# Optimization experiments

Measured on AMD Instinct MI355X. Metric: run time of the kernel, lower is better.

## Reference

```python
import jax, jax.numpy as jnp
import numpy as np

B, NIN, D = 2048, 64, 128
N_LCB, N_FMB, RANK = 32, 32, 24
DIM_HIDDEN = 1024
N_OUT = N_LCB + N_FMB  # == NIN -> identity residual
MAX_VAL = 1.0
EPS_LN_FMB_MIN, EPS_LN_FMB_MAX = 1e-11, 1e7
KERAS_LN_EPS = 1e-3


def setup_inputs() -> dict:
    key = jax.random.key(0)
    ks = jax.random.split(key, 9)
    def w(k, shape, fan):
        return (jax.random.normal(k, shape, jnp.float32) / np.sqrt(fan)).astype(jnp.float32)
    return {
        "x": jax.random.normal(ks[0], (B, NIN, D), jnp.float32),
        "noise": jax.random.uniform(ks[1], (B, N_OUT, D), jnp.float32),
        "w_lcb": w(ks[2], (NIN, N_LCB), NIN),
        "w_rank": w(ks[3], (NIN, RANK), NIN),
        "w1": w(ks[4], (NIN * RANK, DIM_HIDDEN), NIN * RANK),
        "w2": w(ks[5], (DIM_HIDDEN, DIM_HIDDEN), DIM_HIDDEN),
        "w3": w(ks[6], (DIM_HIDDEN, N_FMB * D), DIM_HIDDEN),
        "gamma": jnp.ones((D,), jnp.float32),
        "beta": jnp.zeros((D,), jnp.float32),
    }


def _forward(x, noise, w_lcb, w_rank, w1, w2, w3, gamma, beta):
    # ---- LinearCompressBlock: Dense over feature (emb-count) axis ----
    lcb = jnp.einsum("bnd,nm->bmd", x, w_lcb)  # (B, N_LCB, D)

    # ---- FactorizationMachineBlock ----
    # rank_layer on transposed input: (B, D, NIN) @ (NIN, RANK)
    r = jnp.einsum("bnd,nr->bdr", x, w_rank)          # (B, D, RANK)
    fm = jnp.einsum("bnd,bdr->bnr", x, r)             # (B, NIN, RANK)
    fm = fm.reshape(fm.shape[0], NIN * RANK)
    # custom LayerNorm (no affine, clipped std)
    mu = jnp.mean(fm, axis=-1, keepdims=True)
    cen = fm - mu
    std = jnp.sqrt(jnp.mean(cen * cen, axis=-1, keepdims=True))
    std = jnp.clip(std, EPS_LN_FMB_MIN, EPS_LN_FMB_MAX)
    fm = cen / std
    # MLP: 2 hidden relu layers + linear out, dropout=0 / inference
    h = jax.nn.relu(fm @ w1)
    h = jax.nn.relu(h @ w2)
    fmb = (h @ w3).reshape(-1, N_FMB, D)              # (B, N_FMB, D)

    out = jnp.concatenate((fmb, lcb), axis=1)          # (B, N_OUT, D)
    residual = x                                        # NIN == N_OUT -> identity

    safe = jnp.clip(out, -MAX_VAL, MAX_VAL)
    a = jnp.abs(safe)
    c = lambda t: jnp.clip(t, -MAX_VAL, MAX_VAL)

    # conv term: reshape to (B, N, D//8, 8), 1x1 conv with all-ones (8->8)
    # filter == group-sum broadcast back over the 8 lanes
    g = safe.reshape(safe.shape[0], N_OUT, D // 8, 8)
    conv = jnp.broadcast_to(g.sum(-1, keepdims=True), g.shape).reshape(safe.shape)

    extra = (
        c(jnp.log(a + 1.0))
        + c(jax.lax.rsqrt(a + 1.0))
        + c(jax.nn.softmax(safe, axis=-1))
        + c(jnp.tanh(safe))
        + c(jnp.where(safe >= 0, safe, 0.2 * safe))          # leaky_relu alpha=0.2
        + c(jnp.exp(safe))
        + c(jax.nn.softplus(safe))
        + c(jnp.log1p(a))
        + jnp.zeros_like(safe)                               # zeros_like term
        + c(jnp.round(safe))
        + jnp.ones_like(safe)                                # pow(a+eps, 0) == 1
        + c(jnp.sign(safe))
        + c(jnp.prod(safe, axis=-1, keepdims=True))
        + c(jnp.isnan(safe).astype(jnp.float32))
        + c((~(safe < 0)).astype(jnp.float32))
        + c((safe != 0).astype(jnp.float32))
        + c((safe >= 0).astype(jnp.float32))
        + c(safe.astype(jnp.int8).astype(jnp.float32))       # bitwise_and(x,x)==x after int8 cast
        + c(jnp.max(safe, axis=-1, keepdims=True))
        + c(safe + safe)                                     # add_n([safe, safe])
        + c(safe + safe)                                     # raw Add
        + 7.0 * safe                                         # slice/split-concat/merge/einsum/squeeze/pad/stack identities (|safe|<=1 so clip no-op)
        + c(jnp.where(safe > 0.5, -1.0, safe))               # tensor_scatter_nd_update
        + c(conv)
        + c(noise)                                           # tf.random.uniform (deterministic input)
        + c(jnp.arange(D, dtype=jnp.float32))                # broadcast over last axis
        + c(jnp.sum(safe[0] * safe[0], axis=-1))[None, :, None]  # DiagPart(matmul(safe[0], safe[0]^T))
    )

    pre = out + residual + 1e-10 * extra
    # keras LayerNormalization(axis=-1), default epsilon=1e-3
    m = jnp.mean(pre, axis=-1, keepdims=True)
    v = jnp.mean(jnp.square(pre - m), axis=-1, keepdims=True)
    return (pre - m) * jax.lax.rsqrt(v + KERAS_LN_EPS) * gamma + beta


def reference(x, noise, w_lcb, w_rank, w1, w2, w3, gamma, beta):
    return _forward(x, noise, w_lcb, w_rank, w1, w2, w3, gamma, beta)
```

## Files before the change

### kernel.cpp

```cpp
#include <hip/hip_runtime.h>


typedef _Float16 half8_t __attribute__((ext_vector_type(8)));
typedef _Float16 half4_t __attribute__((ext_vector_type(4)));
typedef float floatx4 __attribute__((ext_vector_type(4)));

#define B_SZ 2048
#define NIN 64
#define D_SZ 128
#define RANK 24
#define FMK (NIN * RANK)
#define HID 1024
#define NFMB_D (32 * 128)
#define ROW_F (NIN * D_SZ)

__device__ __forceinline__ void wg_barrier() {
  asm volatile("s_waitcnt lgkmcnt(0)" ::: "memory");
  __builtin_amdgcn_sched_barrier(0);
  __builtin_amdgcn_s_barrier();
  __builtin_amdgcn_sched_barrier(0);
}

__global__ __launch_bounds__(256) void transpose_cast_all(
    const float* __restrict__ w1, const float* __restrict__ w2,
    const float* __restrict__ w3, const float* __restrict__ w_rank,
    const float* __restrict__ w_lcb, _Float16* __restrict__ w1t,
    _Float16* __restrict__ w2t, _Float16* __restrict__ w3t,
    _Float16* __restrict__ wr16, _Float16* __restrict__ wl16) {
  __shared__ float tile[32][33];
  int bid = blockIdx.x;
  if (bid == 48 * 32 + 32 * 32 + 32 * 128) {
    const int t = threadIdx.x;
#pragma unroll
    for (int k = 0; k < 8; k++) {
      int i = t + k * 256;
      int j = i >> 6, n = i & 63;
      wr16[i] = (_Float16)(j < RANK ? w_rank[n * RANK + j] : 0.f);
      wl16[i] = (_Float16)w_lcb[n * 32 + j];
    }
    return;
  }
  const float* w;
  _Float16* wt;
  int K, N, kt;
  if (bid < 48 * 32) {
    w = w1; wt = w1t; K = FMK; N = HID; kt = 48;
  } else if (bid < 48 * 32 + 32 * 32) {
    bid -= 48 * 32;
    w = w2; wt = w2t; K = HID; N = HID; kt = 32;
  } else {
    bid -= 48 * 32 + 32 * 32;
    w = w3; wt = w3t; K = HID; N = NFMB_D; kt = 32;
  }
  const int tk = (bid % kt) * 32;
  const int tn = (bid / kt) * 32;
  const int tx = threadIdx.x & 31;
  const int ty = threadIdx.x >> 5;
#pragma unroll
  for (int i = 0; i < 4; i++) {
    int k = ty + i * 8;
    tile[k][tx] = w[(size_t)(tk + k) * N + (tn + tx)];
  }
  __syncthreads();
#pragma unroll
  for (int i = 0; i < 4; i++) {
    int n = ty + i * 8;
    wt[(size_t)(tn + n) * K + (tk + tx)] = (_Float16)tile[tx][n];
  }
}

#define STX 72
#define STN 136
__global__ __launch_bounds__(256, 3) void front_kernel(
    const float* __restrict__ x, const _Float16* __restrict__ wr16,
    const _Float16* __restrict__ wl16, const float* __restrict__ gamma,
    const float* __restrict__ beta, _Float16* __restrict__ fmn,
    float* __restrict__ out) {
  constexpr int XT_OFF = 0;
  constexpr int X16_OFF = 18432;
  constexpr int RT_OFF = X16_OFF + 17408;
  constexpr int RED_OFF = RT_OFF + 8704;
  __shared__ __align__(16) char smem[RED_OFF + 32];
  __shared__ float2 lstat[32][4];
  _Float16* xT = (_Float16*)(smem + XT_OFF);
  _Float16* x16 = (_Float16*)(smem + X16_OFF);
  _Float16* rT = (_Float16*)(smem + RT_OFF);
  float* redbuf = (float*)(smem + RED_OFF);
  _Float16* fmn_s = (_Float16*)(smem + RT_OFF);

  const int b = blockIdx.x, t = threadIdx.x;
  const int lane = t & 63;
  const int w = __builtin_amdgcn_readfirstlane(t >> 6);
  const int q = lane >> 4, ln = lane & 15;

  half8_t ar[2][2], al[2][2];
#pragma unroll
  for (int k = 0; k < 2; k++)
#pragma unroll
    for (int mi = 0; mi < 2; mi++) {
      ar[k][mi] = *(const half8_t*)&wr16[(mi * 16 + ln) * 64 + k * 32 + q * 8];
      al[k][mi] = *(const half8_t*)&wl16[(mi * 16 + ln) * 64 + k * 32 + q * 8];
    }

  const float4* xg4 = (const float4*)(x + (size_t)b * ROW_F);
#pragma unroll
  for (int hh = 0; hh < 2; hh++) {
    int bb = t + hh * 256;
    int n0 = (bb >> 5) * 4;
    int bd = bb & 31;
    int d0 = bd * 4;
    float4 L0 = xg4[(n0 + 0) * 32 + bd];
    float4 L1 = xg4[(n0 + 1) * 32 + bd];
    float4 L2 = xg4[(n0 + 2) * 32 + bd];
    float4 L3 = xg4[(n0 + 3) * 32 + bd];
    *(half4_t*)&x16[(n0 + 0) * STN + d0] =
        half4_t{(_Float16)L0.x, (_Float16)L0.y, (_Float16)L0.z, (_Float16)L0.w};
    *(half4_t*)&x16[(n0 + 1) * STN + d0] =
        half4_t{(_Float16)L1.x, (_Float16)L1.y, (_Float16)L1.z, (_Float16)L1.w};
    *(half4_t*)&x16[(n0 + 2) * STN + d0] =
        half4_t{(_Float16)L2.x, (_Float16)L2.y, (_Float16)L2.z, (_Float16)L2.w};
    *(half4_t*)&x16[(n0 + 3) * STN + d0] =
        half4_t{(_Float16)L3.x, (_Float16)L3.y, (_Float16)L3.z, (_Float16)L3.w};
    *(half4_t*)&xT[(d0 + 0) * STX + n0] =
        half4_t{(_Float16)L0.x, (_Float16)L1.x, (_Float16)L2.x, (_Float16)L3.x};
    *(half4_t*)&xT[(d0 + 1) * STX + n0] =
        half4_t{(_Float16)L0.y, (_Float16)L1.y, (_Float16)L2.y, (_Float16)L3.y};
    *(half4_t*)&xT[(d0 + 2) * STX + n0] =
        half4_t{(_Float16)L0.z, (_Float16)L1.z, (_Float16)L2.z, (_Float16)L3.z};
    *(half4_t*)&xT[(d0 + 3) * STX + n0] =
        half4_t{(_Float16)L0.w, (_Float16)L1.w, (_Float16)L2.w, (_Float16)L3.w};
  }
  __syncthreads();

  floatx4 r_acc[2][2] = {};
  floatx4 l_acc[2][2] = {};
#pragma unroll
  for (int k = 0; k < 2; k++) {
    half8_t bfrag[2];
#pragma unroll
    for (int ni = 0; ni < 2; ni++)
      bfrag[ni] =
          *(const half8_t*)&xT[((2 * w + ni) * 16 + ln) * STX + k * 32 + q * 8];
#pragma unroll
    for (int mi = 0; mi < 2; mi++)
#pragma unroll
      for (int ni = 0; ni < 2; ni++) {
        r_acc[mi][ni] = __builtin_amdgcn_mfma_f32_16x16x32_f16(
            ar[k][mi], bfrag[ni], r_acc[mi][ni], 0, 0, 0);
        l_acc[mi][ni] = __builtin_amdgcn_mfma_f32_16x16x32_f16(
            al[k][mi], bfrag[ni], l_acc[mi][ni], 0, 0, 0);
      }
  }
#pragma unroll
  for (int mi = 0; mi < 2; mi++)
#pragma unroll
    for (int ni = 0; ni < 2; ni++)
#pragma unroll
      for (int rr = 0; rr < 4; rr++)
        rT[(mi * 16 + q * 4 + rr) * STN + (2 * w + ni) * 16 + ln] =
            (_Float16)r_acc[mi][ni][rr];
  __syncthreads();

  floatx4 f_acc[2] = {};
#pragma unroll
  for (int k = 0; k < 4; k++) {
    half8_t af = *(const half8_t*)&x16[(w * 16 + ln) * STN + k * 32 + q * 8];
#pragma unroll
    for (int nj = 0; nj < 2; nj++) {
      half8_t bf = *(const half8_t*)&rT[(nj * 16 + ln) * STN + k * 32 + q * 8];
      f_acc[nj] =
          __builtin_amdgcn_mfma_f32_16x16x32_f16(af, bf, f_acc[nj], 0, 0, 0);
    }
  }
  float s = 0.f, s2 = 0.f;
#pragma unroll
  for (int rr = 0; rr < 4; rr++) {
    float v = f_acc[0][rr];
    s += v;
    s2 += v * v;
    float v1 = (ln < 8) ? f_acc[1][rr] : 0.f;
    s += v1;
    s2 += v1 * v1;
  }
#pragma unroll
  for (int off = 1; off < 64; off <<= 1) {
    s += __shfl_xor(s, off);
    s2 += __shfl_xor(s2, off);
  }
  if (lane == 0) {
    redbuf[w * 2] = s;
    redbuf[w * 2 + 1] = s2;
  }
  __syncthreads();
  s = redbuf[0] + redbuf[2] + redbuf[4] + redbuf[6];
  s2 = redbuf[1] + redbuf[3] + redbuf[5] + redbuf[7];
  const float mu = s * (1.f / FMK);
  float var = s2 * (1.f / FMK) - mu * mu;
  var = var > 0.f ? var : 0.f;
  float sd = sqrtf(var);
  sd = sd < 1e-11f ? 1e-11f : (sd > 1e7f ? 1e7f : sd);
  const float inv = 1.f / sd;

#pragma unroll
  for (int nj = 0; nj < 2; nj++) {
    int j = nj * 16 + ln;
    if (j < RANK) {
#pragma unroll
      for (int rr = 0; rr < 4; rr++)
        fmn_s[(w * 16 + q * 4 + rr) * RANK + j] =
            (_Float16)((f_acc[nj][rr] - mu) * inv);
    }
  }

  const int d0 = (2 * w) * 16 + ln;
  const int d1 = d0 + 16;
  const float g0 = gamma[d0], g1 = gamma[d1];
  const float be0 = beta[d0], be1 = beta[d1];
  float lv0[2][4], lv1[2][4];
  float sw[2][4], s2w[2][4];
#pragma unroll
  for (int mi = 0; mi < 2; mi++)
#pragma unroll
    for (int rr = 0; rr < 4; rr++) {
      int m = mi * 16 + q * 4 + rr;
      float v0 = l_acc[mi][0][rr] + (float)x16[(32 + m) * STN + d0];
      float v1 = l_acc[mi][1][rr] + (float)x16[(32 + m) * STN + d1];
      lv0[mi][rr] = v0;
      lv1[mi][rr] = v1;
      sw[mi][rr] = v0 + v1;
      s2w[mi][rr] = v0 * v0 + v1 * v1;
    }
#pragma unroll
  for (int off = 1; off < 16; off <<= 1) {
#pragma unroll
    for (int mi = 0; mi < 2; mi++)
#pragma unroll
      for (int rr = 0; rr < 4; rr++) {
        sw[mi][rr] += __shfl_xor(sw[mi][rr], off);
        s2w[mi][rr] += __shfl_xor(s2w[mi][rr], off);
      }
  }
  if (ln == 0) {
#pragma unroll
    for (int mi = 0; mi < 2; mi++)
#pragma unroll
      for (int rr = 0; rr < 4; rr++)
        lstat[mi * 16 + q * 4 + rr][w] = float2{sw[mi][rr], s2w[mi][rr]};
  }
  __syncthreads();

  half8_t* fg = (half8_t*)(fmn + (size_t)b * FMK);
  if (t < FMK / 8) fg[t] = ((const half8_t*)fmn_s)[t];
  float* ob = out + (size_t)b * ROW_F;
#pragma unroll
  for (int mi = 0; mi < 2; mi++)
#pragma unroll
    for (int rr = 0; rr < 4; rr++) {
      int m = mi * 16 + q * 4 + rr;
      float2 p0 = lstat[m][0], p1 = lstat[m][1];
      float2 p2 = lstat[m][2], p3 = lstat[m][3];
      float S = p0.x + p1.x + p2.x + p3.x;
      float S2 = p0.y + p1.y + p2.y + p3.y;
      float mean = S * (1.f / 128.f);
      float varr = S2 * (1.f / 128.f) - mean * mean;
      float rstd = rsqrtf(varr + 1e-3f);
      ob[(32 + m) * 128 + d0] = (lv0[mi][rr] - mean) * rstd * g0 + be0;
      ob[(32 + m) * 128 + d1] = (lv1[mi][rr] - mean) * rstd * g1 + be1;
    }
}

template <bool RELU>
__global__ __launch_bounds__(256, 2) void gemm_bt(
    const _Float16* __restrict__ A, const _Float16* __restrict__ Bt,
    _Float16* __restrict__ C, int M, int N, int K) {
  constexpr int LDT = 40;
  __shared__ __align__(16) _Float16 As[2][64 * LDT];
  __shared__ __align__(16) _Float16 Bs[2][64 * LDT];
  const int m0 = blockIdx.x * 64;
  const int n0 = blockIdx.y * 64;
  const int t = threadIdx.x;
  const int wave = t >> 6, lane = t & 63;
  const int wr = wave >> 1, wc = wave & 1;
  const int q = lane >> 4, ln = lane & 15;
  const int srow = t >> 2;
  const int skc = t & 3;
  const _Float16* gA = A + (size_t)(m0 + srow) * K + skc * 8;
  const _Float16* gB = Bt + (size_t)(n0 + srow) * K + skc * 8;
  const int ldsw = srow * LDT + skc * 8;
  const int nT = K / 32;

  floatx4 acc[2][2] = {};

  uint4 rax = *(const uint4*)gA;
  uint4 rbx = *(const uint4*)gB;
  *(uint4*)&As[0][ldsw] = rax;
  *(uint4*)&Bs[0][ldsw] = rbx;
  uint4 ray = *(const uint4*)(gA + 32);
  uint4 rby = *(const uint4*)(gB + 32);
  rax = *(const uint4*)(gA + 64);
  rbx = *(const uint4*)(gB + 64);
  wg_barrier();

  for (int tp = 0;;) {
    if (tp + 1 < nT) {
      *(uint4*)&As[1][ldsw] = ray;
      *(uint4*)&Bs[1][ldsw] = rby;
    }
    half8_t af[2], bf[2];
#pragma unroll
    for (int i = 0; i < 2; i++) {
      af[i] = *(const half8_t*)&As[0][(wr * 32 + i * 16 + ln) * LDT + q * 8];
      bf[i] = *(const half8_t*)&Bs[0][(wc * 32 + i * 16 + ln) * LDT + q * 8];
    }
    if (tp + 3 < nT) {
      ray = *(const uint4*)(gA + (tp + 3) * 32);
      rby = *(const uint4*)(gB + (tp + 3) * 32);
    }
#pragma unroll
    for (int i = 0; i < 2; i++)
#pragma unroll
      for (int j = 0; j < 2; j++)
        acc[i][j] = __builtin_amdgcn_mfma_f32_16x16x32_f16(af[i], bf[j],
                                                           acc[i][j], 0, 0, 0);
    if (tp + 1 >= nT) break;
    wg_barrier();
    if (tp + 2 < nT) {
      *(uint4*)&As[0][ldsw] = rax;
      *(uint4*)&Bs[0][ldsw] = rbx;
    }
#pragma unroll
    for (int i = 0; i < 2; i++) {
      af[i] = *(const half8_t*)&As[1][(wr * 32 + i * 16 + ln) * LDT + q * 8];
      bf[i] = *(const half8_t*)&Bs[1][(wc * 32 + i * 16 + ln) * LDT + q * 8];
    }
    if (tp + 4 < nT) {
      rax = *(const uint4*)(gA + (tp + 4) * 32);
      rbx = *(const uint4*)(gB + (tp + 4) * 32);
    }
#pragma unroll
    for (int i = 0; i < 2; i++)
#pragma unroll
      for (int j = 0; j < 2; j++)
        acc[i][j] = __builtin_amdgcn_mfma_f32_16x16x32_f16(af[i], bf[j],
                                                           acc[i][j], 0, 0, 0);
    tp += 2;
    if (tp >= nT) break;
    wg_barrier();
  }

#pragma unroll
  for (int i = 0; i < 2; i++) {
#pragma unroll
    for (int r = 0; r < 4; r++) {
      size_t row = (size_t)(m0 + wr * 32 + i * 16 + q * 4 + r);
      _Float16* crow = C + row * N + n0 + wc * 32 + ln;
#pragma unroll
      for (int j = 0; j < 2; j++) {
        float v = acc[i][j][r];
        if (RELU) v = v > 0.f ? v : 0.f;
        crow[j * 16] = (_Float16)v;
      }
    }
  }
}

__global__ __launch_bounds__(256, 2) void gemm_ln(
    const _Float16* __restrict__ A, const _Float16* __restrict__ Bt,
    const float* __restrict__ x, const float* __restrict__ gamma,
    const float* __restrict__ beta, float* __restrict__ out) {
  constexpr int LDT = 40;
  constexpr int K = HID;
  constexpr int nT = K / 32;
  __shared__ __align__(16) _Float16 As[2][128 * LDT];
  __shared__ __align__(16) _Float16 Bs[2][128 * LDT];
  __shared__ float2 rowst[128][2];
  const int m0 = blockIdx.x * 128;
  const int c = blockIdx.y;
  const int n0 = c * 128;
  const int t = threadIdx.x;
  const int wave = t >> 6, lane = t & 63;
  const int wr = wave >> 1, wc = wave & 1;
  const int q = lane >> 4, ln = lane & 15;
  const int srow = t >> 2;
  const int skc = t & 3;
  const _Float16* gA0 = A + (size_t)(m0 + srow) * K + skc * 8;
  const _Float16* gA1 = gA0 + (size_t)64 * K;
  const _Float16* gB0 = Bt + (size_t)(n0 + srow) * K + skc * 8;
  const _Float16* gB1 = gB0 + (size_t)64 * K;
  const int ldsw = srow * LDT + skc * 8;

  floatx4 acc[4][4] = {};

  uint4 raX0 = *(const uint4*)gA0, raX1 = *(const uint4*)gA1;
  uint4 rbX0 = *(const uint4*)gB0, rbX1 = *(const uint4*)gB1;
  *(uint4*)&As[0][ldsw] = raX0;
  *(uint4*)&As[0][64 * LDT + ldsw] = raX1;
  *(uint4*)&Bs[0][ldsw] = rbX0;
  *(uint4*)&Bs[0][64 * LDT + ldsw] = rbX1;
  uint4 raY0 = *(const uint4*)(gA0 + 32), raY1 = *(const uint4*)(gA1 + 32);
  uint4 rbY0 = *(const uint4*)(gB0 + 32), rbY1 = *(const uint4*)(gB1 + 32);
  raX0 = *(const uint4*)(gA0 + 64);
  raX1 = *(const uint4*)(gA1 + 64);
  rbX0 = *(const uint4*)(gB0 + 64);
  rbX1 = *(const uint4*)(gB1 + 64);

  float xp[4][4][4];
#pragma unroll
  for (int i = 0; i < 4; i++)
#pragma unroll
    for (int r = 0; r < 4; r++) {
      const int row = wr * 64 + i * 16 + q * 4 + r;
      const float* xr = x + (size_t)(m0 + row) * ROW_F + n0 + wc * 64 + ln;
#pragma unroll
      for (int j = 0; j < 4; j++) xp[i][r][j] = xr[j * 16];
    }

  wg_barrier();

  for (int tp = 0;;) {
    if (tp + 1 < nT) {
      *(uint4*)&As[1][ldsw] = raY0;
      *(uint4*)&As[1][64 * LDT + ldsw] = raY1;
      *(uint4*)&Bs[1][ldsw] = rbY0;
      *(uint4*)&Bs[1][64 * LDT + ldsw] = rbY1;
    }
    half8_t af[4], bf[4];
#pragma unroll
    for (int i = 0; i < 4; i++)
      af[i] = *(const half8_t*)&As[0][(wr * 64 + i * 16 + ln) * LDT + q * 8];
#pragma unroll
    for (int j = 0; j < 4; j++)
      bf[j] = *(const half8_t*)&Bs[0][(wc * 64 + j * 16 + ln) * LDT + q * 8];
    if (tp + 3 < nT) {
      raY0 = *(const uint4*)(gA0 + (tp + 3) * 32);
      raY1 = *(const uint4*)(gA1 + (tp + 3) * 32);
      rbY0 = *(const uint4*)(gB0 + (tp + 3) * 32);
      rbY1 = *(const uint4*)(gB1 + (tp + 3) * 32);
    }
#pragma unroll
    for (int i = 0; i < 4; i++)
#pragma unroll
      for (int j = 0; j < 4; j++)
        acc[i][j] = __builtin_amdgcn_mfma_f32_16x16x32_f16(af[i], bf[j],
                                                           acc[i][j], 0, 0, 0);
    if (tp + 1 >= nT) break;
    wg_barrier();
    if (tp + 2 < nT) {
      *(uint4*)&As[0][ldsw] = raX0;
      *(uint4*)&As[0][64 * LDT + ldsw] = raX1;
      *(uint4*)&Bs[0][ldsw] = rbX0;
      *(uint4*)&Bs[0][64 * LDT + ldsw] = rbX1;
    }
#pragma unroll
    for (int i = 0; i < 4; i++)
      af[i] = *(const half8_t*)&As[1][(wr * 64 + i * 16 + ln) * LDT + q * 8];
#pragma unroll
    for (int j = 0; j < 4; j++)
      bf[j] = *(const half8_t*)&Bs[1][(wc * 64 + j * 16 + ln) * LDT + q * 8];
    if (tp + 4 < nT) {
      raX0 = *(const uint4*)(gA0 + (tp + 4) * 32);
      raX1 = *(const uint4*)(gA1 + (tp + 4) * 32);
      rbX0 = *(const uint4*)(gB0 + (tp + 4) * 32);
      rbX1 = *(const uint4*)(gB1 + (tp + 4) * 32);
    }
#pragma unroll
    for (int i = 0; i < 4; i++)
#pragma unroll
      for (int j = 0; j < 4; j++)
        acc[i][j] = __builtin_amdgcn_mfma_f32_16x16x32_f16(af[i], bf[j],
                                                           acc[i][j], 0, 0, 0);
    tp += 2;
    if (tp >= nT) break;
    wg_barrier();
  }

  float s[4][4], s2[4][4];
#pragma unroll
  for (int i = 0; i < 4; i++)
#pragma unroll
    for (int r = 0; r < 4; r++) {
      float ss = 0.f, qq = 0.f;
#pragma unroll
      for (int j = 0; j < 4; j++) {
        float v = acc[i][j][r] + xp[i][r][j];
        acc[i][j][r] = v;
        ss += v;
        qq += v * v;
      }
      s[i][r] = ss;
      s2[i][r] = qq;
    }
#pragma unroll
  for (int off = 1; off < 16; off <<= 1) {
#pragma unroll
    for (int i = 0; i < 4; i++)
#pragma unroll
      for (int r = 0; r < 4; r++) {
        s[i][r] += __shfl_xor(s[i][r], off);
        s2[i][r] += __shfl_xor(s2[i][r], off);
      }
  }
  if (ln == 0) {
#pragma unroll
    for (int i = 0; i < 4; i++)
#pragma unroll
      for (int r = 0; r < 4; r++)
        rowst[wr * 64 + i * 16 + q * 4 + r][wc] = float2{s[i][r], s2[i][r]};
  }
  __syncthreads();
  float g[4], bb[4];
#pragma unroll
  for (int j = 0; j < 4; j++) {
    g[j] = gamma[wc * 64 + j * 16 + ln];
    bb[j] = beta[wc * 64 + j * 16 + ln];
  }
#pragma unroll
  for (int i = 0; i < 4; i++)
#pragma unroll
    for (int r = 0; r < 4; r++) {
      int row = wr * 64 + i * 16 + q * 4 + r;
      float2 p0 = rowst[row][0], p1 = rowst[row][1];
      float mean = (p0.x + p1.x) * (1.f / 128.f);
      float varr = (p0.y + p1.y) * (1.f / 128.f) - mean * mean;
      float rstd = rsqrtf(varr + 1e-3f);
      float* orow = out + (size_t)(m0 + row) * ROW_F + n0 + wc * 64 + ln;
#pragma unroll
      for (int j = 0; j < 4; j++)
        orow[j * 16] = (acc[i][j][r] - mean) * rstd * g[j] + bb[j];
    }
}

extern "C" void kernel_launch(void* const* d_in, const int* in_sizes, int n_in,
                              void* d_out, int out_size, void* d_ws,
                              size_t ws_size, hipStream_t stream) {
  const float* x = (const float*)d_in[0];
  const float* w_lcb = (const float*)d_in[2];
  const float* w_rank = (const float*)d_in[3];
  const float* w1 = (const float*)d_in[4];
  const float* w2 = (const float*)d_in[5];
  const float* w3 = (const float*)d_in[6];
  const float* gamma = (const float*)d_in[7];
  const float* beta = (const float*)d_in[8];
  float* out = (float*)d_out;

  char* ws = (char*)d_ws;
  _Float16* w1t = (_Float16*)ws; ws += (size_t)HID * FMK * 2;
  _Float16* w2t = (_Float16*)ws; ws += (size_t)HID * HID * 2;
  _Float16* w3t = (_Float16*)ws; ws += (size_t)NFMB_D * HID * 2;
  _Float16* fmn = (_Float16*)ws; ws += (size_t)B_SZ * FMK * 2;
  _Float16* h1  = (_Float16*)ws; ws += (size_t)B_SZ * HID * 2;
  _Float16* wr16 = (_Float16*)ws; ws += 32 * 64 * 2;
  _Float16* wl16 = (_Float16*)ws; ws += 32 * 64 * 2;
  _Float16* h2 = fmn;

  transpose_cast_all<<<48 * 32 + 32 * 32 + 32 * 128 + 1, 256, 0, stream>>>(
      w1, w2, w3, w_rank, w_lcb, w1t, w2t, w3t, wr16, wl16);
  front_kernel<<<B_SZ, 256, 0, stream>>>(x, wr16, wl16, gamma, beta, fmn, out);
  gemm_bt<true><<<dim3(B_SZ / 64, HID / 64), 256, 0, stream>>>(
      fmn, w1t, h1, B_SZ, HID, FMK);
  gemm_bt<true><<<dim3(B_SZ / 64, HID / 64), 256, 0, stream>>>(
      h1, w2t, h2, B_SZ, HID, HID);
  gemm_ln<<<dim3(B_SZ / 128, 32), 256, 0, stream>>>(h2, w3t, x, gamma, beta, out);
}
```

Baseline: 254.8 us.

## Deepen gemm K-tile, remap blocks per XCD, and spread residual loads across loop

```diff
diff --git a/kernel.cpp b/kernel.cpp
--- a/kernel.cpp
+++ b/kernel.cpp
@@ -274,10 +274,14 @@
     const _Float16* __restrict__ A, const _Float16* __restrict__ Bt,
     _Float16* __restrict__ C, int M, int N, int K) {
   constexpr int LDT = 40;
-  __shared__ __align__(16) _Float16 As[2][64 * LDT];
-  __shared__ __align__(16) _Float16 Bs[2][64 * LDT];
-  const int m0 = blockIdx.x * 64;
-  const int n0 = blockIdx.y * 64;
+  __shared__ __align__(16) _Float16 As[2][2][64 * LDT];
+  __shared__ __align__(16) _Float16 Bs[2][2][64 * LDT];
+  const int flat = blockIdx.x + (blockIdx.y << 5);
+  const int xcd = flat & 7, sub = flat >> 3;
+  const int mb = sub & 31;
+  const int nb = (xcd << 1) | (sub >> 5);
+  const int m0 = mb * 64;
+  const int n0 = nb * 64;
   const int t = threadIdx.x;
   const int wave = t >> 6, lane = t & 63;
   const int wr = wave >> 1, wc = wave & 1;
@@ -287,62 +291,81 @@
   const _Float16* gA = A + (size_t)(m0 + srow) * K + skc * 8;
   const _Float16* gB = Bt + (size_t)(n0 + srow) * K + skc * 8;
   const int ldsw = srow * LDT + skc * 8;
-  const int nT = K / 32;
+  const int nT = K >> 6;
 
   floatx4 acc[2][2] = {};
 
-  uint4 rax = *(const uint4*)gA;
-  uint4 rbx = *(const uint4*)gB;
-  *(uint4*)&As[0][ldsw] = rax;
-  *(uint4*)&Bs[0][ldsw] = rbx;
-  uint4 ray = *(const uint4*)(gA + 32);
-  uint4 rby = *(const uint4*)(gB + 32);
-  rax = *(const uint4*)(gA + 64);
-  rbx = *(const uint4*)(gB + 64);
+  uint4 raX0 = *(const uint4*)(gA), raX1 = *(const uint4*)(gA + 32);
+  uint4 rbX0 = *(const uint4*)(gB), rbX1 = *(const uint4*)(gB + 32);
+  *(uint4*)&As[0][0][ldsw] = raX0;
+  *(uint4*)&As[0][1][ldsw] = raX1;
+  *(uint4*)&Bs[0][0][ldsw] = rbX0;
+  *(uint4*)&Bs[0][1][ldsw] = rbX1;
+  uint4 raY0 = *(const uint4*)(gA + 64), raY1 = *(const uint4*)(gA + 96);
+  uint4 rbY0 = *(const uint4*)(gB + 64), rbY1 = *(const uint4*)(gB + 96);
+  raX0 = *(const uint4*)(gA + 128);
+  raX1 = *(const uint4*)(gA + 160);
+  rbX0 = *(const uint4*)(gB + 128);
+  rbX1 = *(const uint4*)(gB + 160);
   wg_barrier();
 
   for (int tp = 0;;) {
     if (tp + 1 < nT) {
-      *(uint4*)&As[1][ldsw] = ray;
-      *(uint4*)&Bs[1][ldsw] = rby;
-    }
-    half8_t af[2], bf[2];
-#pragma unroll
-    for (int i = 0; i < 2; i++) {
-      af[i] = *(const half8_t*)&As[0][(wr * 32 + i * 16 + ln) * LDT + q * 8];
-      bf[i] = *(const half8_t*)&Bs[0][(wc * 32 + i * 16 + ln) * LDT + q * 8];
+      *(uint4*)&As[1][0][ldsw] = raY0;
+      *(uint4*)&As[1][1][ldsw] = raY1;
+      *(uint4*)&Bs[1][0][ldsw] = rbY0;
+      *(uint4*)&Bs[1][1][ldsw] = rbY1;
     }
     if (tp + 3 < nT) {
-      ray = *(const uint4*)(gA + (tp + 3) * 32);
-      rby = *(const uint4*)(gB + (tp + 3) * 32);
-    }
-#pragma unroll
-    for (int i = 0; i < 2; i++)
-#pragma unroll
-      for (int j = 0; j < 2; j++)
-        acc[i][j] = __builtin_amdgcn_mfma_f32_16x16x32_f16(af[i], bf[j],
-                                                           acc[i][j], 0, 0, 0);
+      raY0 = *(const uint4*)(gA + (tp + 3) * 64);
+      raY1 = *(const uint4*)(gA + (tp + 3) * 64 + 32);
+      rbY0 = *(const uint4*)(gB + (tp + 3) * 64);
+      rbY1 = *(const uint4*)(gB + (tp + 3) * 64 + 32);
+    }
+#pragma unroll
+    for (int kc = 0; kc < 2; kc++) {
+      half8_t af[2], bf[2];
+#pragma unroll
+      for (int i = 0; i < 2; i++) {
+        af[i] = *(const half8_t*)&As[0][kc][(wr * 32 + i * 16 + ln) * LDT + q * 8];
+        bf[i] = *(const half8_t*)&Bs[0][kc][(wc * 32 + i * 16 + ln) * LDT + q * 8];
+      }
+#pragma unroll
+      for (int i = 0; i < 2; i++)
+#pragma unroll
+        for (int j = 0; j < 2; j++)
+          acc[i][j] = __builtin_amdgcn_mfma_f32_16x16x32_f16(af[i], bf[j],
+                                                             acc[i][j], 0, 0, 0);
+    }
     if (tp + 1 >= nT) break;
     wg_barrier();
     if (tp + 2 < nT) {
-      *(uint4*)&As[0][ldsw] = rax;
-      *(uint4*)&Bs[0][ldsw] = rbx;
-    }
-#pragma unroll
-    for (int i = 0; i < 2; i++) {
-      af[i] = *(const half8_t*)&As[1][(wr * 32 + i * 16 + ln) * LDT + q * 8];
-      bf[i] = *(const half8_t*)&Bs[1][(wc * 32 + i * 16 + ln) * LDT + q * 8];
+      *(uint4*)&As[0][0][ldsw] = raX0;
+      *(uint4*)&As[0][1][ldsw] = raX1;
+      *(uint4*)&Bs[0][0][ldsw] = rbX0;
+      *(uint4*)&Bs[0][1][ldsw] = rbX1;
     }
     if (tp + 4 < nT) {
-      rax = *(const uint4*)(gA + (tp + 4) * 32);
-      rbx = *(const uint4*)(gB + (tp + 4) * 32);
-    }
-#pragma unroll
-    for (int i = 0; i < 2; i++)
-#pragma unroll
-      for (int j = 0; j < 2; j++)
-        acc[i][j] = __builtin_amdgcn_mfma_f32_16x16x32_f16(af[i], bf[j],
-                                                           acc[i][j], 0, 0, 0);
+      raX0 = *(const uint4*)(gA + (tp + 4) * 64);
+      raX1 = *(const uint4*)(gA + (tp + 4) * 64 + 32);
+      rbX0 = *(const uint4*)(gB + (tp + 4) * 64);
+      rbX1 = *(const uint4*)(gB + (tp + 4) * 64 + 32);
+    }
+#pragma unroll
+    for (int kc = 0; kc < 2; kc++) {
+      half8_t af[2], bf[2];
+#pragma unroll
+      for (int i = 0; i < 2; i++) {
+        af[i] = *(const half8_t*)&As[1][kc][(wr * 32 + i * 16 + ln) * LDT + q * 8];
+        bf[i] = *(const half8_t*)&Bs[1][kc][(wc * 32 + i * 16 + ln) * LDT + q * 8];
+      }
+#pragma unroll
+      for (int i = 0; i < 2; i++)
+#pragma unroll
+        for (int j = 0; j < 2; j++)
+          acc[i][j] = __builtin_amdgcn_mfma_f32_16x16x32_f16(af[i], bf[j],
+                                                             acc[i][j], 0, 0, 0);
+    }
     tp += 2;
     if (tp >= nT) break;
     wg_barrier();
@@ -388,8 +411,10 @@
   const _Float16* gB0 = Bt + (size_t)(n0 + srow) * K + skc * 8;
   const _Float16* gB1 = gB0 + (size_t)64 * K;
   const int ldsw = srow * LDT + skc * 8;
+  const float* xbase = x + (size_t)m0 * ROW_F + n0 + wc * 64 + ln;
 
   floatx4 acc[4][4] = {};
+  float xp[4][4][4];
 
   uint4 raX0 = *(const uint4*)gA0, raX1 = *(const uint4*)gA1;
   uint4 rbX0 = *(const uint4*)gB0, rbX1 = *(const uint4*)gB1;
@@ -403,21 +428,11 @@
   raX1 = *(const uint4*)(gA1 + 64);
   rbX0 = *(const uint4*)(gB0 + 64);
   rbX1 = *(const uint4*)(gB1 + 64);
-
-  float xp[4][4][4];
-#pragma unroll
-  for (int i = 0; i < 4; i++)
-#pragma unroll
-    for (int r = 0; r < 4; r++) {
-      const int row = wr * 64 + i * 16 + q * 4 + r;
-      const float* xr = x + (size_t)(m0 + row) * ROW_F + n0 + wc * 64 + ln;
-#pragma unroll
-      for (int j = 0; j < 4; j++) xp[i][r][j] = xr[j * 16];
-    }
-
   wg_barrier();
 
-  for (int tp = 0;;) {
+#pragma unroll
+  for (int p = 0; p < nT / 2; p++) {
+    const int tp = 2 * p;
     if (tp + 1 < nT) {
       *(uint4*)&As[1][ldsw] = raY0;
       *(uint4*)&As[1][64 * LDT + ldsw] = raY1;
@@ -437,13 +452,19 @@
       rbY0 = *(const uint4*)(gB0 + (tp + 3) * 32);
       rbY1 = *(const uint4*)(gB1 + (tp + 3) * 32);
     }
+    {
+      const int xi = p >> 2, xr_ = p & 3;
+      const int row = wr * 64 + xi * 16 + q * 4 + xr_;
+      const float* xr = xbase + (size_t)row * ROW_F;
+#pragma unroll
+      for (int j = 0; j < 4; j++) xp[xi][xr_][j] = xr[j * 16];
+    }
 #pragma unroll
     for (int i = 0; i < 4; i++)
 #pragma unroll
       for (int j = 0; j < 4; j++)
         acc[i][j] = __builtin_amdgcn_mfma_f32_16x16x32_f16(af[i], bf[j],
                                                            acc[i][j], 0, 0, 0);
-    if (tp + 1 >= nT) break;
     wg_barrier();
     if (tp + 2 < nT) {
       *(uint4*)&As[0][ldsw] = raX0;
@@ -469,9 +490,7 @@
       for (int j = 0; j < 4; j++)
         acc[i][j] = __builtin_amdgcn_mfma_f32_16x16x32_f16(af[i], bf[j],
                                                            acc[i][j], 0, 0, 0);
-    tp += 2;
-    if (tp >= nT) break;
-    wg_barrier();
+    if (p < nT / 2 - 1) wg_barrier();
   }
 
   float s[4][4], s2[4][4];
```

Result: faster. 246.9 us (-3.1%).
